# Optimization experiments

Hardware: AMD Instinct MI355X
Metric: run time of the kernel (lower is better)

Reference implementation:

```python
import jax, jax.numpy as jnp
import numpy as np

NUM_HEADS = 4


def setup_inputs() -> dict:
    key = jax.random.key(0)
    ks = jax.random.split(key, 12)
    N, E_edges, ND, ED, D, G = 50000, 800000, 128, 64, 256, 128
    h = jax.random.normal(ks[0], (N, ND), dtype=jnp.float32)
    edge_index = jax.random.randint(ks[1], (2, E_edges), 0, N)
    edge_attr = jax.random.normal(ks[2], (E_edges, ED), dtype=jnp.float32)
    batch = jnp.sort(jax.random.randint(ks[3], (N,), 0, G))
    node_w = jax.random.normal(ks[4], (D, ND), dtype=jnp.float32) / np.sqrt(ND)
    node_b = jnp.zeros((D,), dtype=jnp.float32)
    edge_w = jax.random.normal(ks[5], (D, ED), dtype=jnp.float32) / np.sqrt(ED)
    edge_b = jnp.zeros((D,), dtype=jnp.float32)
    query = jax.random.normal(ks[6], (1, D), dtype=jnp.float32)
    in_w = jax.random.normal(ks[7], (3 * D, D), dtype=jnp.float32) / np.sqrt(D)
    in_b = jnp.zeros((3 * D,), dtype=jnp.float32)
    out_w = jax.random.normal(ks[8], (D, D), dtype=jnp.float32) / np.sqrt(D)
    out_b = jnp.zeros((D,), dtype=jnp.float32)
    return {"h": h, "edge_index": edge_index, "edge_attr": edge_attr, "batch": batch,
            "num_graphs": G, "node_w": node_w, "node_b": node_b,
            "edge_w": edge_w, "edge_b": edge_b, "query": query,
            "in_w": in_w, "in_b": in_b, "out_w": out_w, "out_b": out_b}


def reference(h, edge_index, edge_attr, batch, num_graphs,
              node_w, node_b, edge_w, edge_b, query, in_w, in_b, out_w, out_b):
    N = h.shape[0]
    D = query.shape[-1]
    dh = D // NUM_HEADS
    G = num_graphs
    # node projection
    h_proj = h @ node_w.T + node_b  # [N, D]
    # scatter-mean edge features to source nodes
    row = edge_index[0]
    e_proj = edge_attr @ edge_w.T + edge_b  # [E, D]
    e_sum = jax.ops.segment_sum(e_proj, row, num_segments=N)
    cnt = jax.ops.segment_sum(jnp.ones((row.shape[0],), jnp.float32), row, num_segments=N)
    h_proj = h_proj + e_sum / jnp.maximum(cnt, 1.0)[:, None]
    # per-graph single-query multi-head attention (torch MultiheadAttention math)
    wq, wk, wv = in_w[:D], in_w[D:2 * D], in_w[2 * D:]
    bq, bk, bv = in_b[:D], in_b[D:2 * D], in_b[2 * D:]
    q = (query @ wq.T + bq).reshape(NUM_HEADS, dh)            # [H, dh]
    k = (h_proj @ wk.T + bk).reshape(N, NUM_HEADS, dh)        # [N, H, dh]
    v = (h_proj @ wv.T + bv).reshape(N, NUM_HEADS, dh)        # [N, H, dh]
    scores = jnp.einsum('hd,nhd->nh', q, k) / jnp.sqrt(jnp.float32(dh))  # [N, H]
    smax = jax.ops.segment_max(scores, batch, num_segments=G)  # [G, H]
    w = jnp.exp(scores - smax[batch])                          # [N, H]
    denom = jax.ops.segment_sum(w, batch, num_segments=G)      # [G, H]
    p = w / jnp.maximum(denom[batch], 1e-30)                   # [N, H]
    pooled = jax.ops.segment_sum(p[:, :, None] * v, batch, num_segments=G)  # [G, H, dh]
    out = pooled.reshape(G, 1, D) @ out_w.T + out_b            # [G, 1, D]
    return out
```

## Files before the change

### kernel.cpp

```cpp
#include <hip/hip_runtime.h>
#include <hip/hip_bf16.h>
#include <hip/hip_cooperative_groups.h>
#include <math.h>

namespace cg = cooperative_groups;

#define NDIM 128
#define EDIM 64
#define DDIM 256
#define NSPLIT 4
#define CAP 96
#define AGS 72

typedef __attribute__((ext_vector_type(8))) short short8;

__device__ inline ushort f2bf(float x) {
    uint32_t u = __float_as_uint(x);
    uint32_t r = (u + 0x7fff + ((u >> 16) & 1)) >> 16;
    return (ushort)r;
}
__device__ inline float bf2f(ushort h) { return __uint_as_float(((uint32_t)h) << 16); }

__global__ __launch_bounds__(256, 2) void k_mega(
    const float* __restrict__ h, const int* __restrict__ erow,
    const float* __restrict__ edge_attr, const int* __restrict__ batch,
    const float* __restrict__ node_w, const float* __restrict__ node_b,
    const float* __restrict__ edge_w, const float* __restrict__ edge_b,
    const float* __restrict__ query, const float* __restrict__ in_w,
    const float* __restrict__ in_b, const float* __restrict__ out_w,
    const float* __restrict__ out_b,
    int* __restrict__ fill, float* __restrict__ prep,
    float* __restrict__ pm, float* __restrict__ pdn, float* __restrict__ pe,
    float* __restrict__ pv, float* __restrict__ pu,
    ushort* __restrict__ ebin, float* __restrict__ out,
    int N, int E, int G)
{
    cg::grid_group gridg = cg::this_grid();
    const int tid = threadIdx.x;
    const int bid = blockIdx.x;
    const int gsize = gridDim.x * 256;
    const int gidx = bid * 256 + tid;
    const size_t slab = (size_t)N * EDIM;

    __shared__ float q_s[DDIM], qv[DDIM], qk_s[4 * DDIM], sb_s[4];
    __shared__ ushort agg_s[256 * AGS];
    __shared__ float sc_s[256 * 4], cn_s[256];
    __shared__ float qkn_s[4 * NDIM], qke_s[4 * EDIM], cst[8];
    __shared__ float red_a[16], red_b[16];
    __shared__ float vred[2][4][NDIM], ured[4][4][EDIM];
    __shared__ float vm[4][NDIM], um[4][EDIM];
    __shared__ float scp_s[NSPLIT][4], dnm_s[4], spe_s[4], has_s;
    __shared__ float hb_s[4 * DDIM], po_s[DDIM];

    for (int i = gidx; i < N; i += gsize) fill[i] = 0;
    if (bid == gridDim.x - 1) {
        q_s[tid] = query[tid];
        __syncthreads();
        float acc = in_b[tid];
        const float* wq = in_w + (size_t)tid * DDIM;
        for (int i = 0; i < DDIM; ++i) acc += q_s[i] * wq[i];
        qv[tid] = acc;
        __syncthreads();
        for (int hh = 0; hh < 4; ++hh) {
            float a = 0.f;
            for (int d = 0; d < 64; ++d)
                a += qv[hh * 64 + d] * in_w[(size_t)(DDIM + hh * 64 + d) * DDIM + tid];
            qk_s[hh * DDIM + tid] = a;
        }
        if (tid < 4) {
            float a = 0.f;
            for (int d = 0; d < 64; ++d) a += qv[tid * 64 + d] * in_b[DDIM + tid * 64 + d];
            sb_s[tid] = a;
        }
        __syncthreads();
        for (int idx = tid; idx < 4 * NDIM; idx += 256) {
            int hh = idx >> 7, k = idx & 127;
            float a = 0.f;
            for (int j = 0; j < DDIM; ++j) a += qk_s[hh * DDIM + j] * node_w[(size_t)j * NDIM + k];
            prep[idx] = a;
        }
        {
            int hh = tid >> 6, k = tid & 63;
            float a = 0.f;
            for (int j = 0; j < DDIM; ++j) a += qk_s[hh * DDIM + j] * edge_w[(size_t)j * EDIM + k];
            prep[4 * NDIM + tid] = a;
        }
        if (tid < 4) {
            float a = 0.f, e = 0.f;
            for (int j = 0; j < DDIM; ++j) {
                a += node_b[j] * qk_s[tid * DDIM + j];
                e += edge_b[j] * qk_s[tid * DDIM + j];
            }
            prep[4 * NDIM + 256 + tid] = a + sb_s[tid];
            prep[4 * NDIM + 260 + tid] = e;
        }
    }
    gridg.sync();

    {
        const int total = E * 8;
        for (int it = gidx; it < total; it += gsize) {
            int e = it >> 3;
            int seg8 = it & 7;
            int r = erow[e];
            int pos = 0;
            if (seg8 == 0) pos = atomicAdd(&fill[r], 1);
            pos = __shfl(pos, 0, 8);
            if (pos < CAP) {
                const float* ea = edge_attr + (size_t)e * EDIM + seg8 * 8;
                float4 va = *reinterpret_cast<const float4*>(ea);
                float4 vb = *reinterpret_cast<const float4*>(ea + 4);
                short8 o;
                o[0] = (short)f2bf(va.x); o[1] = (short)f2bf(va.y);
                o[2] = (short)f2bf(va.z); o[3] = (short)f2bf(va.w);
                o[4] = (short)f2bf(vb.x); o[5] = (short)f2bf(vb.y);
                o[6] = (short)f2bf(vb.z); o[7] = (short)f2bf(vb.w);
                *reinterpret_cast<short8*>(
                    ebin + (size_t)pos * slab + (size_t)r * EDIM + seg8 * 8) = o;
            }
        }
    }
    gridg.sync();

    {
        const int gno = bid >> 2;
        const int part = bid & 3;
        const int lane = tid & 63;
        const int wave = tid >> 6;
        const int dv = tid & 127;
        const int g2 = tid >> 7;
        const int du = tid & 63;
        const int g4 = tid >> 6;
        const int seg8 = tid & 7;

        for (int i = tid; i < 4 * NDIM; i += 256) qkn_s[i] = prep[i];
        qke_s[tid] = prep[4 * NDIM + tid];
        if (tid < 8) cst[tid] = prep[4 * NDIM + 256 + tid];
        __syncthreads();

        int lo = 0, hi = N;
        while (lo < hi) { int mid = (lo + hi) >> 1; if (batch[mid] < gno) lo = mid + 1; else hi = mid; }
        const int s = lo;
        hi = N;
        while (lo < hi) { int mid = (lo + hi) >> 1; if (batch[mid] < gno + 1) lo = mid + 1; else hi = mid; }
        const int e = lo;
        const int len = e - s;
        const int cs = s + (len * part) / NSPLIT;
        const int ce = s + (len * (part + 1)) / NSPLIT;

        float m[4], dn[4], spe[4], v[4], uh[4];
#pragma unroll
        for (int hh = 0; hh < 4; ++hh) {
            m[hh] = -INFINITY; dn[hh] = 0.f; spe[hh] = 0.f; v[hh] = 0.f; uh[hh] = 0.f;
        }
        const int hsel = tid & 3;

        for (int c = cs; c < ce; c += 256) {
            int cn = min(256, ce - c);
            __syncthreads();
            if (tid < cn) cn_s[tid] = (float)fill[c + tid];
            __syncthreads();

            for (int pass = 0; pass < 8; ++pass) {
                int node_l = pass * 32 + (tid >> 3);
                if (node_l < cn) {
                    int n = c + node_l;
                    float cntf = cn_s[node_l];
                    int ci = min((int)cntf, CAP);
                    float inv = 1.f / fmaxf(cntf, 1.f);
                    float fl = (cntf > 0.5f) ? 1.f : 0.f;

                    float hd[4] = {0.f, 0.f, 0.f, 0.f};
                    const float4* hp = reinterpret_cast<const float4*>(
                        h + (size_t)n * NDIM + seg8 * 16);
#pragma unroll
                    for (int q = 0; q < 4; ++q) {
                        float4 hv = hp[q];
                        int bq = seg8 * 16 + q * 4;
#pragma unroll
                        for (int hh = 0; hh < 4; ++hh) {
                            const float* qp = &qkn_s[hh * NDIM + bq];
                            hd[hh] += hv.x * qp[0] + hv.y * qp[1] + hv.z * qp[2] + hv.w * qp[3];
                        }
                    }

                    float a[8];
#pragma unroll
                    for (int i = 0; i < 8; ++i) a[i] = 0.f;
                    {
                        const ushort* eb = ebin + (size_t)n * EDIM + seg8 * 8;
                        int j = 0;
                        for (; j + 3 < ci; j += 4) {
                            short8 v0 = *reinterpret_cast<const short8*>(eb + (size_t)(j + 0) * slab);
                            short8 v1 = *reinterpret_cast<const short8*>(eb + (size_t)(j + 1) * slab);
                            short8 v2 = *reinterpret_cast<const short8*>(eb + (size_t)(j + 2) * slab);
                            short8 v3 = *reinterpret_cast<const short8*>(eb + (size_t)(j + 3) * slab);
#pragma unroll
                            for (int i = 0; i < 8; ++i)
                                a[i] += (bf2f((ushort)v0[i]) + bf2f((ushort)v1[i]))
                                      + (bf2f((ushort)v2[i]) + bf2f((ushort)v3[i]));
                        }
                        for (; j < ci; ++j) {
                            short8 v0 = *reinterpret_cast<const short8*>(eb + (size_t)j * slab);
#pragma unroll
                            for (int i = 0; i < 8; ++i) a[i] += bf2f((ushort)v0[i]);
                        }
                    }
                    {
                        short8 o;
#pragma unroll
                        for (int i = 0; i < 8; ++i) o[i] = (short)f2bf(a[i]);
                        *reinterpret_cast<short8*>(&agg_s[node_l * AGS + seg8 * 8]) = o;
                    }
                    float ed[4] = {0.f, 0.f, 0.f, 0.f};
#pragma unroll
                    for (int i = 0; i < 8; ++i) {
#pragma unroll
                        for (int hh = 0; hh < 4; ++hh)
                            ed[hh] += a[i] * qke_s[hh * EDIM + seg8 * 8 + i];
                    }
                    float t[4];
#pragma unroll
                    for (int hh = 0; hh < 4; ++hh) t[hh] = hd[hh] + ed[hh] * inv;
#pragma unroll
                    for (int off = 1; off < 8; off <<= 1) {
#pragma unroll
                        for (int hh = 0; hh < 4; ++hh) t[hh] += __shfl_xor(t[hh], off);
                    }
                    if (seg8 == 0) {
                        float4 sc;
                        sc.x = (t[0] + cst[0] + fl * cst[4]) * 0.125f;
                        sc.y = (t[1] + cst[1] + fl * cst[5]) * 0.125f;
                        sc.z = (t[2] + cst[2] + fl * cst[6]) * 0.125f;
                        sc.w = (t[3] + cst[3] + fl * cst[7]) * 0.125f;
                        *reinterpret_cast<float4*>(&sc_s[node_l * 4]) = sc;
                    }
                }
            }
            __syncthreads();

            float lm = -INFINITY;
            for (int n = tid >> 2; n < cn; n += 64) lm = fmaxf(lm, sc_s[n * 4 + hsel]);
#pragma unroll
            for (int off = 4; off < 64; off <<= 1) lm = fmaxf(lm, __shfl_xor(lm, off));
            if (lane < 4) red_a[wave * 4 + lane] = lm;
            __syncthreads();

            float nm[4];
#pragma unroll
            for (int hh = 0; hh < 4; ++hh) {
                float cm = fmaxf(fmaxf(red_a[hh], red_a[4 + hh]),
                                 fmaxf(red_a[8 + hh], red_a[12 + hh]));
                nm[hh] = fmaxf(m[hh], cm);
                float sc = expf(m[hh] - nm[hh]);
                dn[hh] *= sc; spe[hh] *= sc; v[hh] *= sc; uh[hh] *= sc;
                m[hh] = nm[hh];
            }
            __syncthreads();

            float mh = (hsel == 0) ? nm[0] : (hsel == 1) ? nm[1] : (hsel == 2) ? nm[2] : nm[3];
            float ld = 0.f, le = 0.f;
            for (int idx = tid; idx < cn * 4; idx += 256) {
                float wv = expf(sc_s[idx] - mh);
                sc_s[idx] = wv;
                ld += wv;
                le += wv * ((cn_s[idx >> 2] > 0.5f) ? 1.f : 0.f);
            }
#pragma unroll
            for (int off = 4; off < 64; off <<= 1) {
                ld += __shfl_xor(ld, off);
                le += __shfl_xor(le, off);
            }
            if (lane < 4) { red_a[wave * 4 + lane] = ld; red_b[wave * 4 + lane] = le; }
            __syncthreads();
#pragma unroll
            for (int hh = 0; hh < 4; ++hh) {
                dn[hh]  += red_a[hh] + red_a[4 + hh] + red_a[8 + hh] + red_a[12 + hh];
                spe[hh] += red_b[hh] + red_b[4 + hh] + red_b[8 + hh] + red_b[12 + hh];
            }

            for (int ln = g2; ln < cn; ln += 2) {
                float val = h[(size_t)(c + ln) * NDIM + dv];
                float4 w4 = *reinterpret_cast<const float4*>(&sc_s[ln * 4]);
                v[0] += w4.x * val; v[1] += w4.y * val;
                v[2] += w4.z * val; v[3] += w4.w * val;
            }
            for (int ln = g4; ln < cn; ln += 4) {
                float val = bf2f(agg_s[ln * AGS + du]);
                float ci = 1.f / fmaxf(cn_s[ln], 1.f);
                float4 w4 = *reinterpret_cast<const float4*>(&sc_s[ln * 4]);
                uh[0] += w4.x * ci * val; uh[1] += w4.y * ci * val;
                uh[2] += w4.z * ci * val; uh[3] += w4.w * ci * val;
            }
        }

        __syncthreads();
#pragma unroll
        for (int hh = 0; hh < 4; ++hh) {
            vred[g2][hh][dv] = v[hh];
            ured[g4][hh][du] = uh[hh];
        }
        __syncthreads();

        if (tid < 4) { pm[bid * 4 + tid] = m[tid]; pdn[bid * 4 + tid] = dn[tid]; pe[bid * 4 + tid] = spe[tid]; }
        for (int idx = tid; idx < 4 * NDIM; idx += 256) {
            int hh = idx >> 7, k = idx & 127;
            pv[(size_t)(bid * 4 + hh) * NDIM + k] = vred[0][hh][k] + vred[1][hh][k];
        }
        {
            int hh = tid >> 6, k = tid & 63;
            pu[(size_t)(bid * 4 + hh) * EDIM + k] =
                ured[0][hh][k] + ured[1][hh][k] + ured[2][hh][k] + ured[3][hh][k];
        }
    }
    gridg.sync();

    if (bid < G) {
        const int b0 = NSPLIT * bid;
        if (tid < 4) {
            float Mh = -INFINITY;
#pragma unroll
            for (int p = 0; p < NSPLIT; ++p) Mh = fmaxf(Mh, pm[(b0 + p) * 4 + tid]);
            float d = 0.f, ee = 0.f;
#pragma unroll
            for (int p = 0; p < NSPLIT; ++p) {
                float mp = pm[(b0 + p) * 4 + tid];
                float scp = (mp == -INFINITY) ? 0.f : expf(mp - Mh);
                scp_s[p][tid] = scp;
                d += pdn[(b0 + p) * 4 + tid] * scp;
                ee += pe[(b0 + p) * 4 + tid] * scp;
            }
            dnm_s[tid] = d;
            spe_s[tid] = ee;
            if (tid == 0) has_s = (Mh > -INFINITY) ? 1.f : 0.f;
        }
        __syncthreads();

        for (int idx = tid; idx < 4 * NDIM; idx += 256) {
            int hh = idx >> 7, k = idx & 127;
            float a = 0.f;
#pragma unroll
            for (int p = 0; p < NSPLIT; ++p)
                a += pv[(size_t)((b0 + p) * 4 + hh) * NDIM + k] * scp_s[p][hh];
            vm[hh][k] = a;
        }
        {
            int hh = tid >> 6, k = tid & 63;
            float a = 0.f;
#pragma unroll
            for (int p = 0; p < NSPLIT; ++p)
                a += pu[(size_t)((b0 + p) * 4 + hh) * EDIM + k] * scp_s[p][hh];
            um[hh][k] = a;
        }
        __syncthreads();

        {
            int j = tid;
            float acch[4];
            float nbj = node_b[j], ebj = edge_b[j];
#pragma unroll
            for (int hh = 0; hh < 4; ++hh) acch[hh] = dnm_s[hh] * nbj + spe_s[hh] * ebj;
            const float4* nwr = reinterpret_cast<const float4*>(node_w + (size_t)j * NDIM);
            for (int q = 0; q < NDIM / 4; ++q) {
                float4 w4 = nwr[q];
#pragma unroll
                for (int hh = 0; hh < 4; ++hh) {
                    const float* vp = &vm[hh][q * 4];
                    acch[hh] += w4.x * vp[0] + w4.y * vp[1] + w4.z * vp[2] + w4.w * vp[3];
                }
            }
            const float4* ewr = reinterpret_cast<const float4*>(edge_w + (size_t)j * EDIM);
            for (int q = 0; q < EDIM / 4; ++q) {
                float4 w4 = ewr[q];
#pragma unroll
                for (int hh = 0; hh < 4; ++hh) {
                    const float* up = &um[hh][q * 4];
                    acch[hh] += w4.x * up[0] + w4.y * up[1] + w4.z * up[2] + w4.w * up[3];
                }
            }
#pragma unroll
            for (int hh = 0; hh < 4; ++hh)
                hb_s[hh * DDIM + j] = acch[hh] / fmaxf(dnm_s[hh], 1e-30f);
        }
        __syncthreads();

        const int jh = tid >> 6;
        const float* wv_row = in_w + (size_t)(2 * DDIM + tid) * DDIM;
        const float* hbr = &hb_s[jh * DDIM];
        float p = 0.f;
        for (int i = 0; i < DDIM; i += 4) {
            float4 a = *reinterpret_cast<const float4*>(hbr + i);
            float4 bb = *reinterpret_cast<const float4*>(wv_row + i);
            p += a.x * bb.x + a.y * bb.y + a.z * bb.z + a.w * bb.w;
        }
        p = (p + in_b[2 * DDIM + tid]) * has_s;
        po_s[tid] = p;
        __syncthreads();

        const float* ow_row = out_w + (size_t)tid * DDIM;
        float o = out_b[tid];
        for (int i = 0; i < DDIM; i += 4) {
            float4 a = *reinterpret_cast<const float4*>(&po_s[i]);
            float4 bb = *reinterpret_cast<const float4*>(ow_row + i);
            o += a.x * bb.x + a.y * bb.y + a.z * bb.z + a.w * bb.w;
        }
        out[(size_t)bid * DDIM + tid] = o;
    }
}

__global__ __launch_bounds__(256) void k_setup(
    int* __restrict__ zero_p, int n_zero, int ZBLK,
    const float* __restrict__ node_w, const float* __restrict__ edge_w,
    const float* __restrict__ node_b, const float* __restrict__ edge_b,
    const float* __restrict__ query, const float* __restrict__ in_w,
    const float* __restrict__ in_b, float* __restrict__ prep)
{
    const int tid = threadIdx.x;
    int b = blockIdx.x;
    if (b < ZBLK) {
        int i = b * 256 + tid;
        if (i < n_zero) zero_p[i] = 0;
        return;
    }
    __shared__ float q_s[DDIM];
    __shared__ float qv[DDIM];
    __shared__ float qk_s[4 * DDIM];
    __shared__ float sb_s[4];
    q_s[tid] = query[tid];
    __syncthreads();
    float acc = in_b[tid];
    const float* wq = in_w + (size_t)tid * DDIM;
    for (int i = 0; i < DDIM; ++i) acc += q_s[i] * wq[i];
    qv[tid] = acc;
    __syncthreads();
    for (int h = 0; h < 4; ++h) {
        float a = 0.f;
        for (int d = 0; d < 64; ++d)
            a += qv[h * 64 + d] * in_w[(size_t)(DDIM + h * 64 + d) * DDIM + tid];
        qk_s[h * DDIM + tid] = a;
    }
    if (tid < 4) {
        float a = 0.f;
        for (int d = 0; d < 64; ++d) a += qv[tid * 64 + d] * in_b[DDIM + tid * 64 + d];
        sb_s[tid] = a;
    }
    __syncthreads();
    for (int idx = tid; idx < 4 * NDIM; idx += 256) {
        int hh = idx >> 7, k = idx & 127;
        float a = 0.f;
        for (int j = 0; j < DDIM; ++j) a += qk_s[hh * DDIM + j] * node_w[(size_t)j * NDIM + k];
        prep[idx] = a;
    }
    {
        int hh = tid >> 6, k = tid & 63;
        float a = 0.f;
        for (int j = 0; j < DDIM; ++j) a += qk_s[hh * DDIM + j] * edge_w[(size_t)j * EDIM + k];
        prep[4 * NDIM + tid] = a;
    }
    if (tid < 4) {
        float a = 0.f, e = 0.f;
        for (int j = 0; j < DDIM; ++j) {
            a += node_b[j] * qk_s[tid * DDIM + j];
            e += edge_b[j] * qk_s[tid * DDIM + j];
        }
        prep[4 * NDIM + 256 + tid] = a + sb_s[tid];
        prep[4 * NDIM + 260 + tid] = e;
    }
}

__global__ __launch_bounds__(256) void k_scatbin(
    const int* __restrict__ erow, const float* __restrict__ edge_attr,
    int* __restrict__ fill, ushort* __restrict__ ebin, int E, int N)
{
    const size_t slab = (size_t)N * EDIM;
    int gid = blockIdx.x * 256 + threadIdx.x;
    int e = gid >> 3;
    int seg8 = gid & 7;
    if (e >= E) return;
    int r = erow[e];
    int pos = 0;
    if (seg8 == 0) pos = atomicAdd(&fill[r], 1);
    pos = __shfl(pos, 0, 8);
    if (pos >= CAP) return;
    const float* ea = edge_attr + (size_t)e * EDIM + seg8 * 8;
    float4 va = *reinterpret_cast<const float4*>(ea);
    float4 vb = *reinterpret_cast<const float4*>(ea + 4);
    short8 o;
    o[0] = (short)f2bf(va.x); o[1] = (short)f2bf(va.y);
    o[2] = (short)f2bf(va.z); o[3] = (short)f2bf(va.w);
    o[4] = (short)f2bf(vb.x); o[5] = (short)f2bf(vb.y);
    o[6] = (short)f2bf(vb.z); o[7] = (short)f2bf(vb.w);
    *reinterpret_cast<short8*>(
        ebin + (size_t)pos * slab + (size_t)r * EDIM + seg8 * 8) = o;
}

__global__ __launch_bounds__(256) void k_poolscore(
    const float* __restrict__ h, const ushort* __restrict__ ebin,
    const int* __restrict__ fill, const float* __restrict__ prep,
    const int* __restrict__ batch,
    float* __restrict__ pm, float* __restrict__ pdn, float* __restrict__ pe,
    float* __restrict__ pv, float* __restrict__ pu, int N)
{
    const size_t slab = (size_t)N * EDIM;
    __shared__ ushort agg_s[256 * AGS];
    __shared__ float sc_s[256 * 4];
    __shared__ float cn_s[256];
    __shared__ float qkn_s[4 * NDIM];
    __shared__ float qke_s[4 * EDIM];
    __shared__ float cst[8];
    __shared__ float red_a[16];
    __shared__ float red_b[16];
    __shared__ float vred[2][4][NDIM];
    __shared__ float ured[4][4][EDIM];

    const int b = blockIdx.x;
    const int g = b >> 2;
    const int part = b & 3;
    const int tid = threadIdx.x;
    const int lane = tid & 63;
    const int wave = tid >> 6;
    const int dv = tid & 127;
    const int g2 = tid >> 7;
    const int du = tid & 63;
    const int g4 = tid >> 6;
    const int seg8 = tid & 7;

    for (int i = tid; i < 4 * NDIM; i += 256) qkn_s[i] = prep[i];
    qke_s[tid] = prep[4 * NDIM + tid];
    if (tid < 8) cst[tid] = prep[4 * NDIM + 256 + tid];

    int lo = 0, hi = N;
    while (lo < hi) { int mid = (lo + hi) >> 1; if (batch[mid] < g) lo = mid + 1; else hi = mid; }
    const int s = lo;
    hi = N;
    while (lo < hi) { int mid = (lo + hi) >> 1; if (batch[mid] < g + 1) lo = mid + 1; else hi = mid; }
    const int e = lo;
    const int len = e - s;
    const int cs = s + (len * part) / NSPLIT;
    const int ce = s + (len * (part + 1)) / NSPLIT;

    float m[4], dn[4], spe[4], v[4], uh[4];
#pragma unroll
    for (int hh = 0; hh < 4; ++hh) {
        m[hh] = -INFINITY; dn[hh] = 0.f; spe[hh] = 0.f; v[hh] = 0.f; uh[hh] = 0.f;
    }
    const int hsel = tid & 3;

    for (int c = cs; c < ce; c += 256) {
        int cn = min(256, ce - c);
        __syncthreads();
        if (tid < cn) cn_s[tid] = (float)fill[c + tid];
        __syncthreads();

        for (int pass = 0; pass < 8; ++pass) {
            int node_l = pass * 32 + (tid >> 3);
            if (node_l < cn) {
                int n = c + node_l;
                float cntf = cn_s[node_l];
                int ci = min((int)cntf, CAP);
                float inv = 1.f / fmaxf(cntf, 1.f);
                float fl = (cntf > 0.5f) ? 1.f : 0.f;

                float hd[4] = {0.f, 0.f, 0.f, 0.f};
                const float4* hp = reinterpret_cast<const float4*>(
                    h + (size_t)n * NDIM + seg8 * 16);
#pragma unroll
                for (int q = 0; q < 4; ++q) {
                    float4 hv = hp[q];
                    int bq = seg8 * 16 + q * 4;
#pragma unroll
                    for (int hh = 0; hh < 4; ++hh) {
                        const float* qp = &qkn_s[hh * NDIM + bq];
                        hd[hh] += hv.x * qp[0] + hv.y * qp[1] + hv.z * qp[2] + hv.w * qp[3];
                    }
                }

                float a[8];
#pragma unroll
                for (int i = 0; i < 8; ++i) a[i] = 0.f;
                {
                    const ushort* eb = ebin + (size_t)n * EDIM + seg8 * 8;
                    int j = 0;
                    for (; j + 3 < ci; j += 4) {
                        short8 v0 = *reinterpret_cast<const short8*>(eb + (size_t)(j + 0) * slab);
                        short8 v1 = *reinterpret_cast<const short8*>(eb + (size_t)(j + 1) * slab);
                        short8 v2 = *reinterpret_cast<const short8*>(eb + (size_t)(j + 2) * slab);
                        short8 v3 = *reinterpret_cast<const short8*>(eb + (size_t)(j + 3) * slab);
#pragma unroll
                        for (int i = 0; i < 8; ++i)
                            a[i] += (bf2f((ushort)v0[i]) + bf2f((ushort)v1[i]))
                                  + (bf2f((ushort)v2[i]) + bf2f((ushort)v3[i]));
                    }
                    for (; j < ci; ++j) {
                        short8 v0 = *reinterpret_cast<const short8*>(eb + (size_t)j * slab);
#pragma unroll
                        for (int i = 0; i < 8; ++i) a[i] += bf2f((ushort)v0[i]);
                    }
                }
                {
                    short8 o;
#pragma unroll
                    for (int i = 0; i < 8; ++i) o[i] = (short)f2bf(a[i]);
                    *reinterpret_cast<short8*>(&agg_s[node_l * AGS + seg8 * 8]) = o;
                }
                float ed[4] = {0.f, 0.f, 0.f, 0.f};
#pragma unroll
                for (int i = 0; i < 8; ++i) {
#pragma unroll
                    for (int hh = 0; hh < 4; ++hh)
                        ed[hh] += a[i] * qke_s[hh * EDIM + seg8 * 8 + i];
                }
                float t[4];
#pragma unroll
                for (int hh = 0; hh < 4; ++hh) t[hh] = hd[hh] + ed[hh] * inv;
#pragma unroll
                for (int off = 1; off < 8; off <<= 1) {
#pragma unroll
                    for (int hh = 0; hh < 4; ++hh) t[hh] += __shfl_xor(t[hh], off);
                }
                if (seg8 == 0) {
                    float4 sc;
                    sc.x = (t[0] + cst[0] + fl * cst[4]) * 0.125f;
                    sc.y = (t[1] + cst[1] + fl * cst[5]) * 0.125f;
                    sc.z = (t[2] + cst[2] + fl * cst[6]) * 0.125f;
                    sc.w = (t[3] + cst[3] + fl * cst[7]) * 0.125f;
                    *reinterpret_cast<float4*>(&sc_s[node_l * 4]) = sc;
                }
            }
        }
        __syncthreads();

        float lm = -INFINITY;
        for (int n = tid >> 2; n < cn; n += 64) lm = fmaxf(lm, sc_s[n * 4 + hsel]);
#pragma unroll
        for (int off = 4; off < 64; off <<= 1) lm = fmaxf(lm, __shfl_xor(lm, off));
        if (lane < 4) red_a[wave * 4 + lane] = lm;
        __syncthreads();

        float nm[4];
#pragma unroll
        for (int hh = 0; hh < 4; ++hh) {
            float cm = fmaxf(fmaxf(red_a[hh], red_a[4 + hh]),
                             fmaxf(red_a[8 + hh], red_a[12 + hh]));
            nm[hh] = fmaxf(m[hh], cm);
            float sc = expf(m[hh] - nm[hh]);
            dn[hh] *= sc; spe[hh] *= sc; v[hh] *= sc; uh[hh] *= sc;
            m[hh] = nm[hh];
        }
        __syncthreads();

        float mh = (hsel == 0) ? nm[0] : (hsel == 1) ? nm[1] : (hsel == 2) ? nm[2] : nm[3];
        float ld = 0.f, le = 0.f;
        for (int idx = tid; idx < cn * 4; idx += 256) {
            float wv = expf(sc_s[idx] - mh);
            sc_s[idx] = wv;
            ld += wv;
            le += wv * ((cn_s[idx >> 2] > 0.5f) ? 1.f : 0.f);
        }
#pragma unroll
        for (int off = 4; off < 64; off <<= 1) {
            ld += __shfl_xor(ld, off);
            le += __shfl_xor(le, off);
        }
        if (lane < 4) { red_a[wave * 4 + lane] = ld; red_b[wave * 4 + lane] = le; }
        __syncthreads();
#pragma unroll
        for (int hh = 0; hh < 4; ++hh) {
            dn[hh]  += red_a[hh] + red_a[4 + hh] + red_a[8 + hh] + red_a[12 + hh];
            spe[hh] += red_b[hh] + red_b[4 + hh] + red_b[8 + hh] + red_b[12 + hh];
        }

        for (int ln = g2; ln < cn; ln += 2) {
            float val = h[(size_t)(c + ln) * NDIM + dv];
            float4 w4 = *reinterpret_cast<const float4*>(&sc_s[ln * 4]);
            v[0] += w4.x * val; v[1] += w4.y * val;
            v[2] += w4.z * val; v[3] += w4.w * val;
        }
        for (int ln = g4; ln < cn; ln += 4) {
            float val = bf2f(agg_s[ln * AGS + du]);
            float ci = 1.f / fmaxf(cn_s[ln], 1.f);
            float4 w4 = *reinterpret_cast<const float4*>(&sc_s[ln * 4]);
            uh[0] += w4.x * ci * val; uh[1] += w4.y * ci * val;
            uh[2] += w4.z * ci * val; uh[3] += w4.w * ci * val;
        }
    }

    __syncthreads();
#pragma unroll
    for (int hh = 0; hh < 4; ++hh) {
        vred[g2][hh][dv] = v[hh];
        ured[g4][hh][du] = uh[hh];
    }
    __syncthreads();

    if (tid < 4) { pm[b * 4 + tid] = m[tid]; pdn[b * 4 + tid] = dn[tid]; pe[b * 4 + tid] = spe[tid]; }
    for (int idx = tid; idx < 4 * NDIM; idx += 256) {
        int hh = idx >> 7, k = idx & 127;
        pv[(size_t)(b * 4 + hh) * NDIM + k] = vred[0][hh][k] + vred[1][hh][k];
    }
    {
        int hh = tid >> 6, k = tid & 63;
        pu[(size_t)(b * 4 + hh) * EDIM + k] =
            ured[0][hh][k] + ured[1][hh][k] + ured[2][hh][k] + ured[3][hh][k];
    }
}

__global__ __launch_bounds__(256) void k_out(
    const float* __restrict__ pm, const float* __restrict__ pdn, const float* __restrict__ pe,
    const float* __restrict__ pv, const float* __restrict__ pu,
    const float* __restrict__ node_w, const float* __restrict__ edge_w,
    const float* __restrict__ node_b, const float* __restrict__ edge_b,
    const float* __restrict__ in_w, const float* __restrict__ in_b,
    const float* __restrict__ out_w, const float* __restrict__ out_b,
    float* __restrict__ out)
{
    __shared__ float vm[4][NDIM];
    __shared__ float um[4][EDIM];
    __shared__ float scp_s[NSPLIT][4];
    __shared__ float dnm_s[4];
    __shared__ float spe_s[4];
    __shared__ float has_s;
    __shared__ float hb_s[4 * DDIM];
    __shared__ float po_s[DDIM];

    const int g = blockIdx.x;
    const int tid = threadIdx.x;
    const int b0 = NSPLIT * g;

    if (tid < 4) {
        float Mh = -INFINITY;
#pragma unroll
        for (int p = 0; p < NSPLIT; ++p) Mh = fmaxf(Mh, pm[(b0 + p) * 4 + tid]);
        float d = 0.f, ee = 0.f;
#pragma unroll
        for (int p = 0; p < NSPLIT; ++p) {
            float mp = pm[(b0 + p) * 4 + tid];
            float scp = (mp == -INFINITY) ? 0.f : expf(mp - Mh);
            scp_s[p][tid] = scp;
            d += pdn[(b0 + p) * 4 + tid] * scp;
            ee += pe[(b0 + p) * 4 + tid] * scp;
        }
        dnm_s[tid] = d;
        spe_s[tid] = ee;
        if (tid == 0) has_s = (Mh > -INFINITY) ? 1.f : 0.f;
    }
    __syncthreads();

    for (int idx = tid; idx < 4 * NDIM; idx += 256) {
        int hh = idx >> 7, k = idx & 127;
        float a = 0.f;
#pragma unroll
        for (int p = 0; p < NSPLIT; ++p)
            a += pv[(size_t)((b0 + p) * 4 + hh) * NDIM + k] * scp_s[p][hh];
        vm[hh][k] = a;
    }
    {
        int hh = tid >> 6, k = tid & 63;
        float a = 0.f;
#pragma unroll
        for (int p = 0; p < NSPLIT; ++p)
            a += pu[(size_t)((b0 + p) * 4 + hh) * EDIM + k] * scp_s[p][hh];
        um[hh][k] = a;
    }
    __syncthreads();

    {
        int j = tid;
        float acch[4];
        float nbj = node_b[j], ebj = edge_b[j];
#pragma unroll
        for (int hh = 0; hh < 4; ++hh) acch[hh] = dnm_s[hh] * nbj + spe_s[hh] * ebj;
        const float4* nwr = reinterpret_cast<const float4*>(node_w + (size_t)j * NDIM);
        for (int q = 0; q < NDIM / 4; ++q) {
            float4 w4 = nwr[q];
#pragma unroll
            for (int hh = 0; hh < 4; ++hh) {
                const float* vp = &vm[hh][q * 4];
                acch[hh] += w4.x * vp[0] + w4.y * vp[1] + w4.z * vp[2] + w4.w * vp[3];
            }
        }
        const float4* ewr = reinterpret_cast<const float4*>(edge_w + (size_t)j * EDIM);
        for (int q = 0; q < EDIM / 4; ++q) {
            float4 w4 = ewr[q];
#pragma unroll
            for (int hh = 0; hh < 4; ++hh) {
                const float* up = &um[hh][q * 4];
                acch[hh] += w4.x * up[0] + w4.y * up[1] + w4.z * up[2] + w4.w * up[3];
            }
        }
#pragma unroll
        for (int hh = 0; hh < 4; ++hh)
            hb_s[hh * DDIM + j] = acch[hh] / fmaxf(dnm_s[hh], 1e-30f);
    }
    __syncthreads();

    const int jh = tid >> 6;
    const float* wv_row = in_w + (size_t)(2 * DDIM + tid) * DDIM;
    const float* hbr = &hb_s[jh * DDIM];
    float p = 0.f;
    for (int i = 0; i < DDIM; i += 4) {
        float4 a = *reinterpret_cast<const float4*>(hbr + i);
        float4 bb = *reinterpret_cast<const float4*>(wv_row + i);
        p += a.x * bb.x + a.y * bb.y + a.z * bb.z + a.w * bb.w;
    }
    p = (p + in_b[2 * DDIM + tid]) * has_s;
    po_s[tid] = p;
    __syncthreads();

    const float* ow_row = out_w + (size_t)tid * DDIM;
    float o = out_b[tid];
    for (int i = 0; i < DDIM; i += 4) {
        float4 a = *reinterpret_cast<const float4*>(&po_s[i]);
        float4 bb = *reinterpret_cast<const float4*>(ow_row + i);
        o += a.x * bb.x + a.y * bb.y + a.z * bb.z + a.w * bb.w;
    }
    out[(size_t)g * DDIM + tid] = o;
}

extern "C" void kernel_launch(void* const* d_in, const int* in_sizes, int n_in,
                              void* d_out, int out_size, void* d_ws, size_t ws_size,
                              hipStream_t stream) {
    const float* h         = (const float*)d_in[0];
    const int*   edge_idx  = (const int*)d_in[1];
    const float* edge_attr = (const float*)d_in[2];
    const int*   batch     = (const int*)d_in[3];
    const float* node_w    = (const float*)d_in[5];
    const float* node_b    = (const float*)d_in[6];
    const float* edge_w    = (const float*)d_in[7];
    const float* edge_b    = (const float*)d_in[8];
    const float* query     = (const float*)d_in[9];
    const float* in_w      = (const float*)d_in[10];
    const float* in_b      = (const float*)d_in[11];
    const float* out_w     = (const float*)d_in[12];
    const float* out_b     = (const float*)d_in[13];
    float* out = (float*)d_out;

    int N = in_sizes[0] / NDIM;
    int E = in_sizes[2] / EDIM;
    int G = out_size / DDIM;

    char* ws = (char*)d_ws;
    size_t off = 0;
    auto alloc = [&](size_t bytes) { void* p = ws + off; off += (bytes + 255) & ~(size_t)255; return p; };

    int*    fill    = (int*)alloc((size_t)N * 4);
    float*  prep    = (float*)alloc(776 * 4);
    float*  pm      = (float*)alloc((size_t)NSPLIT * G * 4 * 4);
    float*  pdn     = (float*)alloc((size_t)NSPLIT * G * 4 * 4);
    float*  pe      = (float*)alloc((size_t)NSPLIT * G * 4 * 4);
    float*  pv      = (float*)alloc((size_t)NSPLIT * G * 4 * NDIM * 4);
    float*  pu      = (float*)alloc((size_t)NSPLIT * G * 4 * EDIM * 4);
    ushort* ebin    = (ushort*)alloc((size_t)N * CAP * EDIM * 2);

    int nblk = 0;
    hipError_t qerr = hipOccupancyMaxActiveBlocksPerMultiprocessor(&nblk, k_mega, 256, 0);
    hipDeviceProp_t props;
    int dev = 0;
    hipGetDevice(&dev);
    hipGetDeviceProperties(&props, dev);
    const int grid_blocks = NSPLIT * G;
    bool coop_ok = (qerr == hipSuccess) &&
                   ((long long)nblk * props.multiProcessorCount >= grid_blocks) &&
                   props.cooperativeLaunch;

    if (coop_ok) {
        void* args[] = {
            (void*)&h, (void*)&edge_idx, (void*)&edge_attr, (void*)&batch,
            (void*)&node_w, (void*)&node_b, (void*)&edge_w, (void*)&edge_b,
            (void*)&query, (void*)&in_w, (void*)&in_b, (void*)&out_w, (void*)&out_b,
            (void*)&fill, (void*)&prep, (void*)&pm, (void*)&pdn, (void*)&pe,
            (void*)&pv, (void*)&pu, (void*)&ebin, (void*)&out,
            (void*)&N, (void*)&E, (void*)&G
        };
        hipError_t lerr = hipLaunchCooperativeKernel(
            k_mega, dim3(grid_blocks), dim3(256), args, 0, stream);
        if (lerr == hipSuccess) return;
    }

    const int ZBLK = (N + 255) / 256;
    k_setup<<<ZBLK + 1, 256, 0, stream>>>(
        fill, N, ZBLK, node_w, edge_w, node_b, edge_b, query, in_w, in_b, prep);
    k_scatbin<<<((E * 8) + 255) / 256, 256, 0, stream>>>(
        edge_idx, edge_attr, fill, ebin, E, N);
    k_poolscore<<<NSPLIT * G, 256, 0, stream>>>(
        h, ebin, fill, prep, batch, pm, pdn, pe, pv, pu, N);
    k_out<<<G, 256, 0, stream>>>(
        pm, pdn, pe, pv, pu, node_w, edge_w, node_b, edge_b,
        in_w, in_b, out_w, out_b, out);
}
```

Baseline: 184.5 us.

## Double graph split count, halve node chunk, alias shared memory to raise occupancy

Splits each graph across 8 blocks instead of 4 and processes nodes in chunks of 128 instead of 256, shrinking the per-block shared buffers. Phase-specific shared arrays are overlaid onto one union buffer, and the launch bound asks for 4 blocks per SM instead of 2. The aim is more resident blocks and a larger cooperative grid to hide gather latency, at the cost of more partial results to merge and tighter register limits.

New measurement: 190.2 us. 3.1% more time.

```diff
diff --git a/kernel.cpp b/kernel.cpp
--- a/kernel.cpp
+++ b/kernel.cpp
@@ -8,9 +8,10 @@
 #define NDIM 128
 #define EDIM 64
 #define DDIM 256
-#define NSPLIT 4
+#define NSPLIT 8
 #define CAP 96
 #define AGS 72
+#define CHUNK 128
 
 typedef __attribute__((ext_vector_type(8))) short short8;
 
@@ -21,7 +22,7 @@
 }
 __device__ inline float bf2f(ushort h) { return __uint_as_float(((uint32_t)h) << 16); }
 
-__global__ __launch_bounds__(256, 2) void k_mega(
+__global__ __launch_bounds__(256, 4) void k_mega(
     const float* __restrict__ h, const int* __restrict__ erow,
     const float* __restrict__ edge_attr, const int* __restrict__ batch,
     const float* __restrict__ node_w, const float* __restrict__ node_b,
@@ -42,18 +43,18 @@
     const int gidx = bid * 256 + tid;
     const size_t slab = (size_t)N * EDIM;
 
-    __shared__ float q_s[DDIM], qv[DDIM], qk_s[4 * DDIM], sb_s[4];
-    __shared__ ushort agg_s[256 * AGS];
-    __shared__ float sc_s[256 * 4], cn_s[256];
+    __shared__ __align__(16) char uni[CHUNK * AGS * 2];
+    __shared__ float sc_s[CHUNK * 4], cn_s[CHUNK];
     __shared__ float qkn_s[4 * NDIM], qke_s[4 * EDIM], cst[8];
     __shared__ float red_a[16], red_b[16];
     __shared__ float vred[2][4][NDIM], ured[4][4][EDIM];
-    __shared__ float vm[4][NDIM], um[4][EDIM];
-    __shared__ float scp_s[NSPLIT][4], dnm_s[4], spe_s[4], has_s;
-    __shared__ float hb_s[4 * DDIM], po_s[DDIM];
 
     for (int i = gidx; i < N; i += gsize) fill[i] = 0;
     if (bid == gridDim.x - 1) {
+        float* q_s  = (float*)uni;
+        float* qv   = q_s + DDIM;
+        float* qk_s = qv + DDIM;
+        float* sb_s = qk_s + 4 * DDIM;
         q_s[tid] = query[tid];
         __syncthreads();
         float acc = in_b[tid];
@@ -123,8 +124,9 @@
     gridg.sync();
 
     {
-        const int gno = bid >> 2;
-        const int part = bid & 3;
+        ushort* agg_s = (ushort*)uni;
+        const int gno = bid >> 3;
+        const int part = bid & 7;
         const int lane = tid & 63;
         const int wave = tid >> 6;
         const int dv = tid & 127;
@@ -155,13 +157,13 @@
         }
         const int hsel = tid & 3;
 
-        for (int c = cs; c < ce; c += 256) {
-            int cn = min(256, ce - c);
+        for (int c = cs; c < ce; c += CHUNK) {
+            int cn = min(CHUNK, ce - c);
             __syncthreads();
             if (tid < cn) cn_s[tid] = (float)fill[c + tid];
             __syncthreads();
 
-            for (int pass = 0; pass < 8; ++pass) {
+            for (int pass = 0; pass < CHUNK / 32; ++pass) {
                 int node_l = pass * 32 + (tid >> 3);
                 if (node_l < cn) {
                     int n = c + node_l;
@@ -316,6 +318,15 @@
     gridg.sync();
 
     if (bid < G) {
+        float* vm    = (float*)uni;
+        float* um    = vm + 4 * NDIM;
+        float* hb_s  = um + 4 * EDIM;
+        float* po_s  = hb_s + 4 * DDIM;
+        float* scp_s = po_s + DDIM;
+        float* dnm_s = scp_s + NSPLIT * 4;
+        float* spe_s = dnm_s + 4;
+        float* has_s = spe_s + 4;
+
         const int b0 = NSPLIT * bid;
         if (tid < 4) {
             float Mh = -INFINITY;
@@ -326,13 +337,13 @@
             for (int p = 0; p < NSPLIT; ++p) {
                 float mp = pm[(b0 + p) * 4 + tid];
                 float scp = (mp == -INFINITY) ? 0.f : expf(mp - Mh);
-                scp_s[p][tid] = scp;
+                scp_s[p * 4 + tid] = scp;
                 d += pdn[(b0 + p) * 4 + tid] * scp;
                 ee += pe[(b0 + p) * 4 + tid] * scp;
             }
             dnm_s[tid] = d;
             spe_s[tid] = ee;
-            if (tid == 0) has_s = (Mh > -INFINITY) ? 1.f : 0.f;
+            if (tid == 0) has_s[0] = (Mh > -INFINITY) ? 1.f : 0.f;
         }
         __syncthreads();
 
@@ -341,16 +352,16 @@
             float a = 0.f;
 #pragma unroll
             for (int p = 0; p < NSPLIT; ++p)
-                a += pv[(size_t)((b0 + p) * 4 + hh) * NDIM + k] * scp_s[p][hh];
-            vm[hh][k] = a;
+                a += pv[(size_t)((b0 + p) * 4 + hh) * NDIM + k] * scp_s[p * 4 + hh];
+            vm[hh * NDIM + k] = a;
         }
         {
             int hh = tid >> 6, k = tid & 63;
             float a = 0.f;
 #pragma unroll
             for (int p = 0; p < NSPLIT; ++p)
-                a += pu[(size_t)((b0 + p) * 4 + hh) * EDIM + k] * scp_s[p][hh];
-            um[hh][k] = a;
+                a += pu[(size_t)((b0 + p) * 4 + hh) * EDIM + k] * scp_s[p * 4 + hh];
+            um[hh * EDIM + k] = a;
         }
         __syncthreads();
 
@@ -365,7 +376,7 @@
                 float4 w4 = nwr[q];
 #pragma unroll
                 for (int hh = 0; hh < 4; ++hh) {
-                    const float* vp = &vm[hh][q * 4];
+                    const float* vp = &vm[hh * NDIM + q * 4];
                     acch[hh] += w4.x * vp[0] + w4.y * vp[1] + w4.z * vp[2] + w4.w * vp[3];
                 }
             }
@@ -374,7 +385,7 @@
                 float4 w4 = ewr[q];
 #pragma unroll
                 for (int hh = 0; hh < 4; ++hh) {
-                    const float* up = &um[hh][q * 4];
+                    const float* up = &um[hh * EDIM + q * 4];
                     acch[hh] += w4.x * up[0] + w4.y * up[1] + w4.z * up[2] + w4.w * up[3];
                 }
             }
@@ -393,7 +404,7 @@
             float4 bb = *reinterpret_cast<const float4*>(wv_row + i);
             p += a.x * bb.x + a.y * bb.y + a.z * bb.z + a.w * bb.w;
         }
-        p = (p + in_b[2 * DDIM + tid]) * has_s;
+        p = (p + in_b[2 * DDIM + tid]) * has_s[0];
         po_s[tid] = p;
         __syncthreads();
 
@@ -502,9 +513,9 @@
     float* __restrict__ pv, float* __restrict__ pu, int N)
 {
     const size_t slab = (size_t)N * EDIM;
-    __shared__ ushort agg_s[256 * AGS];
-    __shared__ float sc_s[256 * 4];
-    __shared__ float cn_s[256];
+    __shared__ ushort agg_s[CHUNK * AGS];
+    __shared__ float sc_s[CHUNK * 4];
+    __shared__ float cn_s[CHUNK];
     __shared__ float qkn_s[4 * NDIM];
     __shared__ float qke_s[4 * EDIM];
     __shared__ float cst[8];
@@ -514,8 +525,8 @@
     __shared__ float ured[4][4][EDIM];
 
     const int b = blockIdx.x;
-    const int g = b >> 2;
-    const int part = b & 3;
+    const int g = b >> 3;
+    const int part = b & 7;
     const int tid = threadIdx.x;
     const int lane = tid & 63;
     const int wave = tid >> 6;
@@ -546,13 +557,13 @@
     }
     const int hsel = tid & 3;
 
-    for (int c = cs; c < ce; c += 256) {
-        int cn = min(256, ce - c);
+    for (int c = cs; c < ce; c += CHUNK) {
+        int cn = min(CHUNK, ce - c);
         __syncthreads();
         if (tid < cn) cn_s[tid] = (float)fill[c + tid];
         __syncthreads();
 
-        for (int pass = 0; pass < 8; ++pass) {
+        for (int pass = 0; pass < CHUNK / 32; ++pass) {
             int node_l = pass * 32 + (tid >> 3);
             if (node_l < cn) {
                 int n = c + node_l;
```
